# Kernel optimization log

Hardware: AMD Instinct MI355X
Metric: run time of the kernel (lower is better)

## Reference

```python
import jax, jax.numpy as jnp
import numpy as np

B, S, HID = 2, 2048, 1024
NH = 16
DK = HID // NH


def setup_inputs() -> dict:
    key0 = jax.random.key(0)
    ks = jax.random.split(key0, 16)
    inp = {
        "query": jax.random.normal(ks[0], (B, S, HID), dtype=jnp.float32),
        "key": jax.random.normal(ks[1], (B, S, HID), dtype=jnp.float32),
        "value": jax.random.normal(ks[2], (B, S, HID), dtype=jnp.float32),
        "bias": jax.random.uniform(ks[3], (B, S), dtype=jnp.float32),
        "mask": jax.random.randint(ks[4], (B, 1, S), 0, 2, dtype=jnp.int32),
        "wq": jax.random.normal(ks[5], (HID, HID), dtype=jnp.float32) * 0.02,
        "bq": jax.random.normal(ks[6], (HID,), dtype=jnp.float32) * 0.02,
        "wk": jax.random.normal(ks[7], (HID, HID), dtype=jnp.float32) * 0.02,
        "bk": jax.random.normal(ks[8], (HID,), dtype=jnp.float32) * 0.02,
        "wv": jax.random.normal(ks[9], (HID, HID), dtype=jnp.float32) * 0.02,
        "bv": jax.random.normal(ks[10], (HID,), dtype=jnp.float32) * 0.02,
        "wo": jax.random.normal(ks[11], (HID, HID), dtype=jnp.float32) * 0.02,
        "bo": jax.random.normal(ks[12], (HID,), dtype=jnp.float32) * 0.02,
    }
    return inp


def reference(query, key, value, bias, mask, wq, bq, wk, bk, wv, bv, wo, bo):
    b, s, hid = query.shape
    # attn_bias_type == 'both': gate K and V with per-token scalar bias
    # (dropout is eval-mode identity): x + p[..., None] * x
    key = key + bias[:, :, None] * key
    value = value + bias[:, :, None] * value

    def proj(x, w, bb):
        # torch Linear: x @ W.T + b, then split heads -> [b, nh, s, dk]
        y = x @ w.T + bb
        return y.reshape(b, s, NH, DK).transpose(0, 2, 1, 3)

    q = proj(query, wq, bq)
    k = proj(key, wk, bk)
    v = proj(value, wv, bv)

    scores = jnp.einsum("bhqd,bhkd->bhqk", q, k) / jnp.sqrt(jnp.asarray(DK, q.dtype))
    m = mask[:, None]  # [b,1,1,s] broadcast over heads and query positions
    scores = jnp.where(m == 0, jnp.asarray(-10000.0, scores.dtype), scores)
    p_attn = jax.nn.softmax(scores, axis=-1)
    x = jnp.einsum("bhqk,bhkd->bhqd", p_attn, v)
    x = x.transpose(0, 2, 1, 3).reshape(b, s, hid)
    return x @ wo.T + bo
```

## Files before the change

### kernel.cpp

```cpp
#include <hip/hip_runtime.h>
#include <stdint.h>

#define NB   2
#define SS   2048
#define HIDN 1024
#define NHEAD 16
#define DKK  64

typedef __attribute__((ext_vector_type(8))) short bf16x8;
typedef __attribute__((ext_vector_type(4))) float f32x4;

__device__ __forceinline__ uint16_t f2bf(float f) {
    uint32_t u = __float_as_uint(f);
    u += 0x7FFF + ((u >> 16) & 1);
    return (uint16_t)(u >> 16);
}
__device__ __forceinline__ uint32_t pk2(float f0, float f1) {
    uint32_t u0 = __float_as_uint(f0);
    uint32_t u1 = __float_as_uint(f1);
    u0 += 0x7FFF + ((u0 >> 16) & 1);
    u1 += 0x7FFF + ((u1 >> 16) & 1);
    return (u0 >> 16) | (u1 & 0xFFFF0000u);
}
__device__ __forceinline__ uint32_t cvtpk(float lo, float hi) {
    uint32_t r;
    asm("v_cvt_pk_bf16_f32 %0, %1, %2" : "=v"(r) : "v"(lo), "v"(hi));
    return r;
}
__device__ __forceinline__ float exp2_fast(float x) {
    float r;
    asm("v_exp_f32 %0, %1" : "=v"(r) : "v"(x));
    return r;
}
__device__ __forceinline__ uint4 pack8(const float* __restrict__ s, float sc) {
    float4 a = *(const float4*)s;
    float4 b = *(const float4*)(s + 4);
    uint4 r;
    r.x = pk2(sc * a.x, sc * a.y);
    r.y = pk2(sc * a.z, sc * a.w);
    r.z = pk2(sc * b.x, sc * b.y);
    r.w = pk2(sc * b.z, sc * b.w);
    return r;
}
__device__ __forceinline__ void gl_lds16(const uint16_t* g, uint16_t* l) {
    __builtin_amdgcn_global_load_lds((const __attribute__((address_space(1))) void*)g,
                                     (__attribute__((address_space(3))) void*)l,
                                     16, 0, 0);
}

__global__ __launch_bounds__(256, 4)
void cvt_all(const float* __restrict__ q, const float* __restrict__ k,
             const float* __restrict__ v, const float* __restrict__ bias,
             const float* __restrict__ w0, const float* __restrict__ w1,
             const float* __restrict__ w2, const float* __restrict__ w3,
             uint16_t* __restrict__ q16, uint16_t* __restrict__ k16,
             uint16_t* __restrict__ v16, uint16_t* __restrict__ w16o)
{
    int i = blockIdx.x * 256 + threadIdx.x;
    if (i < 524288) {
        size_t e = (size_t)i * 8;
        float sc = 1.0f + bias[i >> 7];
        *(uint4*)(q16 + e) = pack8(q + e, 1.0f);
        *(uint4*)(k16 + e) = pack8(k + e, sc);
        *(uint4*)(v16 + e) = pack8(v + e, sc);
    } else {
        int j = i - 524288;
        const float* src = (j < 131072) ? w0 : (j < 262144) ? w1
                         : (j < 393216) ? w2 : w3;
        size_t e = (size_t)(j & 131071) * 8;
        *(uint4*)(w16o + (size_t)(j >> 17) * 1048576 + e) = pack8(src + e, 1.0f);
    }
}

__device__ __forceinline__ void gemm_core(const uint16_t* __restrict__ A,
                                          const uint16_t* __restrict__ W,
                                          uint16_t* __restrict__ As0,
                                          uint16_t* __restrict__ As1,
                                          uint16_t* __restrict__ Bs0,
                                          uint16_t* __restrict__ Bs1,
                                          int m0, int n0,
                                          f32x4 acc[4][4])
{
    const int t    = threadIdx.x;
    const int w    = t >> 6;
    const int lane = t & 63;
    const int q    = lane >> 4;
    const int lr   = lane & 15;
    const int wr   = (w >> 1) * 64;
    const int wc   = (w & 1) * 64;
    const int srow = lane >> 3;
    const int sg   = (lane & 7) ^ srow;

#pragma unroll
    for (int c = 0; c < 4; ++c) {
        int r = w * 32 + c * 8;
        gl_lds16(A + (size_t)(m0 + r + srow) * HIDN + sg * 8, As0 + r * 64);
        gl_lds16(W + (size_t)(n0 + r + srow) * HIDN + sg * 8, Bs0 + r * 64);
    }

    for (int it = 0; it < 16; ++it) {
        uint16_t* Asc = (it & 1) ? As1 : As0;
        uint16_t* Bsc = (it & 1) ? Bs1 : Bs0;
        uint16_t* Asn = (it & 1) ? As0 : As1;
        uint16_t* Bsn = (it & 1) ? Bs0 : Bs1;
        __syncthreads();
        if (it + 1 < 16) {
            int k0 = (it + 1) * 64;
#pragma unroll
            for (int c = 0; c < 4; ++c) {
                int r = w * 32 + c * 8;
                gl_lds16(A + (size_t)(m0 + r + srow) * HIDN + k0 + sg * 8,
                         Asn + r * 64);
                gl_lds16(W + (size_t)(n0 + r + srow) * HIDN + k0 + sg * 8,
                         Bsn + r * 64);
            }
        }
        bf16x8 af[2][4], bfr[2][4];
#pragma unroll
        for (int s = 0; s < 2; ++s) {
#pragma unroll
            for (int i = 0; i < 4; ++i)
                af[s][i] = *(const bf16x8*)&Asc[(wr + i * 16 + lr) * 64 +
                                                (((s * 4 + q) ^ (lr & 7)) * 8)];
#pragma unroll
            for (int j = 0; j < 4; ++j)
                bfr[s][j] = *(const bf16x8*)&Bsc[(wc + j * 16 + lr) * 64 +
                                                 (((s * 4 + q) ^ (lr & 7)) * 8)];
        }
#pragma unroll
        for (int s = 0; s < 2; ++s)
#pragma unroll
            for (int i = 0; i < 4; ++i)
#pragma unroll
                for (int j = 0; j < 4; ++j)
                    acc[i][j] = __builtin_amdgcn_mfma_f32_16x16x32_bf16(
                        af[s][i], bfr[s][j], acc[i][j], 0, 0, 0);
    }
}

__global__ __launch_bounds__(256, 2)
void gemm_qkv(const uint16_t* __restrict__ Qin, const uint16_t* __restrict__ Kin,
              const uint16_t* __restrict__ Vin, const uint16_t* __restrict__ W16,
              const float* __restrict__ bq, const float* __restrict__ bk,
              const float* __restrict__ bv,
              uint16_t* __restrict__ Qb, uint16_t* __restrict__ Kb,
              uint16_t* __restrict__ Vtb)
{
    __shared__ __align__(16) uint16_t As[2][128 * 64];
    __shared__ __align__(16) uint16_t Bs[2][128 * 64];

    const int bid = (blockIdx.z << 8) | (blockIdx.y << 3) | blockIdx.x;
    const int swz = (bid & 7) * 96 + (bid >> 3);
    const int z   = swz >> 8;
    const int m0  = ((swz >> 3) & 31) * 128;
    const int n0  = (swz & 7) * 128;

    const uint16_t* A    = (z == 0) ? Qin : (z == 1) ? Kin : Vin;
    const uint16_t* W    = W16 + (size_t)z * 1048576;
    const float*    bias = (z == 0) ? bq : (z == 1) ? bk : bv;
    const float     osc  = (z == 0) ? 0.125f * 1.44269504f : 1.0f;

    const int t    = threadIdx.x;
    const int w    = t >> 6;
    const int lane = t & 63;
    const int q    = lane >> 4;
    const int lr   = lane & 15;
    const int wr   = (w >> 1) * 64;
    const int wc   = (w & 1) * 64;

    f32x4 acc[4][4] = {};
    gemm_core(A, W, As[0], As[1], Bs[0], Bs[1], m0, n0, acc);

    if (z < 2) {
        uint16_t* o = (z == 0) ? Qb : Kb;
#pragma unroll
        for (int i = 0; i < 4; ++i)
#pragma unroll
            for (int j = 0; j < 4; ++j) {
                int gn = n0 + wc + j * 16 + lr;
                float bvx = bias[gn];
#pragma unroll
                for (int r = 0; r < 4; ++r) {
                    int row = m0 + wr + i * 16 + q * 4 + r;
                    int b = row >> 11, s = row & 2047;
                    size_t dst = (size_t)b * (NHEAD * SS * DKK)
                               + (size_t)(gn >> 6) * (SS * DKK)
                               + (size_t)s * DKK + (gn & 63);
                    o[dst] = f2bf((acc[i][j][r] + bvx) * osc);
                }
            }
    } else {
        __syncthreads();
        uint16_t* Tr = As[0];
        int b = m0 >> 11;
#pragma unroll
        for (int hh = 0; hh < 2; ++hh) {
            if ((w & 1) == hh) {
#pragma unroll
                for (int j = 0; j < 4; ++j) {
                    int dl = j * 16 + lr;
                    float bvx = bias[n0 + hh * 64 + dl];
#pragma unroll
                    for (int r = 0; r < 4; ++r) {
                        int sl = wr + (q * 4 + r);
                        Tr[dl * 136 + sl +  0] = f2bf(acc[0][j][r] + bvx);
                        Tr[dl * 136 + sl + 16] = f2bf(acc[1][j][r] + bvx);
                        Tr[dl * 136 + sl + 32] = f2bf(acc[2][j][r] + bvx);
                        Tr[dl * 136 + sl + 48] = f2bf(acc[3][j][r] + bvx);
                    }
                }
            }
            __syncthreads();
            int hgl = (n0 >> 6) + hh;
#pragma unroll
            for (int p = 0; p < 4; ++p) {
                int idx = p * 256 + t;
                int d   = idx >> 4;
                int sc8 = (idx & 15) * 8;
                size_t dst = ((size_t)(b * NHEAD + hgl) * DKK + d) * SS
                           + (m0 & 2047) + sc8;
                *(uint4*)&Vtb[dst] = *(const uint4*)&Tr[d * 136 + sc8];
            }
            __syncthreads();
        }
    }
}

__global__ __launch_bounds__(256, 2)
void gemm_out(const uint16_t* __restrict__ Xb, const uint16_t* __restrict__ W,
              const float* __restrict__ bias, float* __restrict__ out)
{
    __shared__ __align__(16) uint16_t As[2][128 * 64];
    __shared__ __align__(16) uint16_t Bs[2][128 * 64];

    const int bid = (blockIdx.y << 3) | blockIdx.x;
    const int swz = (bid & 7) * 32 + (bid >> 3);
    const int m0  = (swz >> 3) * 128;
    const int n0  = (swz & 7) * 128;

    const int t    = threadIdx.x;
    const int w    = t >> 6;
    const int lane = t & 63;
    const int q    = lane >> 4;
    const int lr   = lane & 15;
    const int wr   = (w >> 1) * 64;
    const int wc   = (w & 1) * 64;

    f32x4 acc[4][4] = {};
    gemm_core(Xb, W, As[0], As[1], Bs[0], Bs[1], m0, n0, acc);

#pragma unroll
    for (int i = 0; i < 4; ++i)
#pragma unroll
        for (int j = 0; j < 4; ++j) {
            int gn = n0 + wc + j * 16 + lr;
            float bvx = bias[gn];
#pragma unroll
            for (int r = 0; r < 4; ++r) {
                int row = m0 + wr + i * 16 + q * 4 + r;
                out[(size_t)row * HIDN + gn] = acc[i][j][r] + bvx;
            }
        }
}

__global__ __launch_bounds__(512, 4)
void flash_attn(const uint16_t* __restrict__ Qg, const uint16_t* __restrict__ Kg,
                const uint16_t* __restrict__ Vtg, const int* __restrict__ mask,
                uint16_t* __restrict__ X)
{
    __shared__ __align__(16) uint16_t QP[128 * 64];
    __shared__ __align__(16) uint16_t Ks[64 * 64];
    __shared__ __align__(16) uint16_t Vs[64 * 64];
    __shared__ __align__(16) float Amf[SS];

    const int t    = threadIdx.x;
    const int w    = t >> 6;
    const int lane = t & 63;
    const int q    = lane >> 4;
    const int lr   = lane & 15;

    const int bid = (blockIdx.y << 4) | blockIdx.x;
    const int swz = (bid & 7) * 64 + (bid >> 3);
    const int bh  = swz >> 4;
    const int q0  = (swz & 15) * 128;

    const int b    = bh >> 4;
    const int h    = bh & 15;
    const size_t head = (size_t)bh * SS * DKK;

#pragma unroll
    for (int p = 0; p < 2; ++p) {
        int idx = p * 512 + t;
        int row = idx >> 3;
        int g   = idx & 7;
        *(uint4*)&QP[row * 64 + ((g ^ (row & 7)) * 8)] =
            *(const uint4*)(Qg + head + (size_t)(q0 + row) * DKK + g * 8);
    }
#pragma unroll
    for (int p = 0; p < 4; ++p) {
        int i = p * 512 + t;
        Amf[i] = (mask[b * SS + i] == 0) ? -14426.95f : 0.0f;
    }

    const int srow = t >> 3;
    const int sgf  = t & 7;
    const int scol = sgf * 8;
    const int swzc = (sgf ^ (srow & 7)) * 8;
    uint4 kreg = *(const uint4*)(Kg + head + (size_t)srow * DKK + scol);
    uint4 vreg = *(const uint4*)(Vtg + head + (size_t)srow * SS + scol);

    __syncthreads();

    bf16x8 qf[2];
#pragma unroll
    for (int s = 0; s < 2; ++s)
        qf[s] = *(const bf16x8*)&QP[(w * 16 + lr) * 64 +
                                    (((s * 4 + q) ^ (lr & 7)) * 8)];

    float mst = -1e30f, lst = 0.0f;
    f32x4 oacc[4] = {};

    for (int kv0 = 0; kv0 < SS; kv0 += 64) {
        *(uint4*)&Ks[srow * 64 + swzc] = kreg;
        *(uint4*)&Vs[srow * 64 + swzc] = vreg;
        __syncthreads();

        if (kv0 + 64 < SS) {
            kreg = *(const uint4*)(Kg + head + (size_t)(kv0 + 64 + srow) * DKK + scol);
            vreg = *(const uint4*)(Vtg + head + (size_t)srow * SS + kv0 + 64 + scol);
        }

        f32x4 st[4];
#pragma unroll
        for (int ni = 0; ni < 4; ++ni) {
            bf16x8 kf0 = *(const bf16x8*)&Ks[(ni * 16 + lr) * 64 +
                                             ((q ^ (lr & 7)) * 8)];
            bf16x8 kf1 = *(const bf16x8*)&Ks[(ni * 16 + lr) * 64 +
                                             (((4 + q) ^ (lr & 7)) * 8)];
            f32x4 z = {0.0f, 0.0f, 0.0f, 0.0f};
            z = __builtin_amdgcn_mfma_f32_16x16x32_bf16(kf0, qf[0], z, 0, 0, 0);
            z = __builtin_amdgcn_mfma_f32_16x16x32_bf16(kf1, qf[1], z, 0, 0, 0);
            st[ni] = z;
        }

        float rmax = -1e30f;
#pragma unroll
        for (int ni = 0; ni < 4; ++ni) {
            float4 am = *(const float4*)&Amf[kv0 + ni * 16 + q * 4];
            st[ni][0] += am.x; st[ni][1] += am.y;
            st[ni][2] += am.z; st[ni][3] += am.w;
#pragma unroll
            for (int r = 0; r < 4; ++r) rmax = fmaxf(rmax, st[ni][r]);
        }
        rmax = fmaxf(rmax, __shfl_xor(rmax, 16));
        rmax = fmaxf(rmax, __shfl_xor(rmax, 32));

        if (__any(rmax > mst + 11.5f)) {
            float mnew  = fmaxf(mst, rmax);
            float alpha = exp2_fast(mst - mnew);
            mst = mnew;
            lst *= alpha;
#pragma unroll
            for (int dj = 0; dj < 4; ++dj) {
                oacc[dj][0] *= alpha; oacc[dj][1] *= alpha;
                oacc[dj][2] *= alpha; oacc[dj][3] *= alpha;
            }
        }

        float rsum = 0.0f;
#pragma unroll
        for (int ni = 0; ni < 4; ++ni) {
            float p0 = exp2_fast(st[ni][0] - mst);
            float p1 = exp2_fast(st[ni][1] - mst);
            float p2 = exp2_fast(st[ni][2] - mst);
            float p3 = exp2_fast(st[ni][3] - mst);
            rsum += (p0 + p1) + (p2 + p3);
            uint2 pw = make_uint2(cvtpk(p0, p1), cvtpk(p2, p3));
            *(uint2*)&QP[(w * 16 + lr) * 64 +
                         (((ni * 2 + (q >> 1)) ^ (lr & 7)) * 8) + (q & 1) * 4] = pw;
        }
        lst += rsum;

#pragma unroll
        for (int ks = 0; ks < 2; ++ks) {
            bf16x8 pfB = *(const bf16x8*)&QP[(w * 16 + lr) * 64 +
                                             (((ks * 4 + q) ^ (lr & 7)) * 8)];
#pragma unroll
            for (int dj = 0; dj < 4; ++dj) {
                bf16x8 vfA = *(const bf16x8*)&Vs[(dj * 16 + lr) * 64 +
                                                 (((ks * 4 + q) ^ (lr & 7)) * 8)];
                oacc[dj] = __builtin_amdgcn_mfma_f32_16x16x32_bf16(vfA, pfB, oacc[dj], 0, 0, 0);
            }
        }
        __syncthreads();
    }

    {
        lst += __shfl_xor(lst, 16);
        lst += __shfl_xor(lst, 32);
        float inv = 1.0f / lst;
        int s = q0 + w * 16 + lr;
        uint16_t* xp = X + (size_t)(b * SS + s) * HIDN + h * DKK;
#pragma unroll
        for (int dj = 0; dj < 4; ++dj) {
            uint2 pw = make_uint2(cvtpk(oacc[dj][0] * inv, oacc[dj][1] * inv),
                                  cvtpk(oacc[dj][2] * inv, oacc[dj][3] * inv));
            *(uint2*)(xp + dj * 16 + q * 4) = pw;
        }
    }
}

extern "C" void kernel_launch(void* const* d_in, const int* in_sizes, int n_in,
                              void* d_out, int out_size, void* d_ws, size_t ws_size,
                              hipStream_t stream) {
    const float* query = (const float*)d_in[0];
    const float* key   = (const float*)d_in[1];
    const float* value = (const float*)d_in[2];
    const float* bias  = (const float*)d_in[3];
    const int*   mask  = (const int*)d_in[4];
    const float* wq = (const float*)d_in[5];
    const float* bq = (const float*)d_in[6];
    const float* wk = (const float*)d_in[7];
    const float* bk = (const float*)d_in[8];
    const float* wv = (const float*)d_in[9];
    const float* bv = (const float*)d_in[10];
    const float* wo = (const float*)d_in[11];
    const float* bo = (const float*)d_in[12];

    const size_t TEN = (size_t)NB * SS * HIDN;
    uint16_t* Qin = (uint16_t*)d_ws;
    uint16_t* Kin = Qin + TEN;
    uint16_t* Vin = Kin + TEN;
    uint16_t* W16 = Vin + TEN;
    uint16_t* Qb  = W16 + 4 * 1048576;
    uint16_t* Kb  = Qb + TEN;
    uint16_t* Vtb = Kb + TEN;
    uint16_t* Xb  = Qin;

    cvt_all<<<4096, 256, 0, stream>>>(query, key, value, bias,
                                      wq, wk, wv, wo, Qin, Kin, Vin, W16);
    gemm_qkv<<<dim3(8, 32, 3), 256, 0, stream>>>(Qin, Kin, Vin, W16,
                                                 bq, bk, bv, Qb, Kb, Vtb);
    flash_attn<<<dim3(SS / 128, NB * NHEAD), 512, 0, stream>>>(Qb, Kb, Vtb, mask, Xb);
    gemm_out<<<dim3(8, 32), 256, 0, stream>>>(Xb, W16 + 3 * 1048576, bo, (float*)d_out);
}
```

Baseline: 231.4 us.

## Single-buffer GEMM LDS tiles to raise occupancy in projection kernels

```diff
diff --git a/kernel.cpp b/kernel.cpp
--- a/kernel.cpp
+++ b/kernel.cpp
@@ -74,10 +74,8 @@
 
 __device__ __forceinline__ void gemm_core(const uint16_t* __restrict__ A,
                                           const uint16_t* __restrict__ W,
-                                          uint16_t* __restrict__ As0,
-                                          uint16_t* __restrict__ As1,
-                                          uint16_t* __restrict__ Bs0,
-                                          uint16_t* __restrict__ Bs1,
+                                          uint16_t* __restrict__ As,
+                                          uint16_t* __restrict__ Bs,
                                           int m0, int n0,
                                           f32x4 acc[4][4])
 {
@@ -91,54 +89,41 @@
     const int srow = lane >> 3;
     const int sg   = (lane & 7) ^ srow;
 
-#pragma unroll
-    for (int c = 0; c < 4; ++c) {
-        int r = w * 32 + c * 8;
-        gl_lds16(A + (size_t)(m0 + r + srow) * HIDN + sg * 8, As0 + r * 64);
-        gl_lds16(W + (size_t)(n0 + r + srow) * HIDN + sg * 8, Bs0 + r * 64);
-    }
-
     for (int it = 0; it < 16; ++it) {
-        uint16_t* Asc = (it & 1) ? As1 : As0;
-        uint16_t* Bsc = (it & 1) ? Bs1 : Bs0;
-        uint16_t* Asn = (it & 1) ? As0 : As1;
-        uint16_t* Bsn = (it & 1) ? Bs0 : Bs1;
+        const int k0 = it * 64;
+#pragma unroll
+        for (int c = 0; c < 4; ++c) {
+            int r = w * 32 + c * 8;
+            gl_lds16(A + (size_t)(m0 + r + srow) * HIDN + k0 + sg * 8,
+                     As + r * 64);
+            gl_lds16(W + (size_t)(n0 + r + srow) * HIDN + k0 + sg * 8,
+                     Bs + r * 64);
+        }
         __syncthreads();
-        if (it + 1 < 16) {
-            int k0 = (it + 1) * 64;
-#pragma unroll
-            for (int c = 0; c < 4; ++c) {
-                int r = w * 32 + c * 8;
-                gl_lds16(A + (size_t)(m0 + r + srow) * HIDN + k0 + sg * 8,
-                         Asn + r * 64);
-                gl_lds16(W + (size_t)(n0 + r + srow) * HIDN + k0 + sg * 8,
-                         Bsn + r * 64);
-            }
-        }
-        bf16x8 af[2][4], bfr[2][4];
+
 #pragma unroll
         for (int s = 0; s < 2; ++s) {
+            bf16x8 af[4], bfr[4];
 #pragma unroll
             for (int i = 0; i < 4; ++i)
-                af[s][i] = *(const bf16x8*)&Asc[(wr + i * 16 + lr) * 64 +
-                                                (((s * 4 + q) ^ (lr & 7)) * 8)];
+                af[i] = *(const bf16x8*)&As[(wr + i * 16 + lr) * 64 +
+                                            (((s * 4 + q) ^ (lr & 7)) * 8)];
 #pragma unroll
             for (int j = 0; j < 4; ++j)
-                bfr[s][j] = *(const bf16x8*)&Bsc[(wc + j * 16 + lr) * 64 +
-                                                 (((s * 4 + q) ^ (lr & 7)) * 8)];
-        }
-#pragma unroll
-        for (int s = 0; s < 2; ++s)
+                bfr[j] = *(const bf16x8*)&Bs[(wc + j * 16 + lr) * 64 +
+                                             (((s * 4 + q) ^ (lr & 7)) * 8)];
 #pragma unroll
             for (int i = 0; i < 4; ++i)
 #pragma unroll
                 for (int j = 0; j < 4; ++j)
                     acc[i][j] = __builtin_amdgcn_mfma_f32_16x16x32_bf16(
-                        af[s][i], bfr[s][j], acc[i][j], 0, 0, 0);
-    }
-}
-
-__global__ __launch_bounds__(256, 2)
+                        af[i], bfr[j], acc[i][j], 0, 0, 0);
+        }
+        __syncthreads();
+    }
+}
+
+__global__ __launch_bounds__(256, 3)
 void gemm_qkv(const uint16_t* __restrict__ Qin, const uint16_t* __restrict__ Kin,
               const uint16_t* __restrict__ Vin, const uint16_t* __restrict__ W16,
               const float* __restrict__ bq, const float* __restrict__ bk,
@@ -146,8 +131,9 @@
               uint16_t* __restrict__ Qb, uint16_t* __restrict__ Kb,
               uint16_t* __restrict__ Vtb)
 {
-    __shared__ __align__(16) uint16_t As[2][128 * 64];
-    __shared__ __align__(16) uint16_t Bs[2][128 * 64];
+    __shared__ __align__(16) uint16_t Sh[2 * 128 * 64];
+    uint16_t* As = Sh;
+    uint16_t* Bs = Sh + 128 * 64;
 
     const int bid = (blockIdx.z << 8) | (blockIdx.y << 3) | blockIdx.x;
     const int swz = (bid & 7) * 96 + (bid >> 3);
@@ -169,7 +155,7 @@
     const int wc   = (w & 1) * 64;
 
     f32x4 acc[4][4] = {};
-    gemm_core(A, W, As[0], As[1], Bs[0], Bs[1], m0, n0, acc);
+    gemm_core(A, W, As, Bs, m0, n0, acc);
 
     if (z < 2) {
         uint16_t* o = (z == 0) ? Qb : Kb;
@@ -190,8 +176,7 @@
                 }
             }
     } else {
-        __syncthreads();
-        uint16_t* Tr = As[0];
+        uint16_t* Tr = Sh;
         int b = m0 >> 11;
 #pragma unroll
         for (int hh = 0; hh < 2; ++hh) {
@@ -226,12 +211,13 @@
     }
 }
 
-__global__ __launch_bounds__(256, 2)
+__global__ __launch_bounds__(256, 3)
 void gemm_out(const uint16_t* __restrict__ Xb, const uint16_t* __restrict__ W,
               const float* __restrict__ bias, float* __restrict__ out)
 {
-    __shared__ __align__(16) uint16_t As[2][128 * 64];
-    __shared__ __align__(16) uint16_t Bs[2][128 * 64];
+    __shared__ __align__(16) uint16_t Sh[2 * 128 * 64];
+    uint16_t* As = Sh;
+    uint16_t* Bs = Sh + 128 * 64;
 
     const int bid = (blockIdx.y << 3) | blockIdx.x;
     const int swz = (bid & 7) * 32 + (bid >> 3);
@@ -247,7 +233,7 @@
     const int wc   = (w & 1) * 64;
 
     f32x4 acc[4][4] = {};
-    gemm_core(Xb, W, As[0], As[1], Bs[0], Bs[1], m0, n0, acc);
+    gemm_core(Xb, W, As, Bs, m0, n0, acc);
 
 #pragma unroll
     for (int i = 0; i < 4; ++i)
```

Measured after the change: 227.4 us. Within noise of the previous version (-1.8%).
